# Performance work log

Hardware: AMD Instinct MI355X
Metric: run time of the kernel (lower is better)

## Reference

```python
import jax, jax.numpy as jnp
import numpy as np

NUM_BLOCKS = 16  # 4x4 grid of 2x2 blocks over the 8x8 matrix
E_BLK, H_BLK = 4, 2
E_CROSS, H_CROSS = 64, 8
VOCAB = 32000
LN_EPS = 1e-5


def _mha(x, Wqkv, bqkv, Wo, bo, nheads):
    """torch nn.MultiheadAttention (batch_first, self-attn, eval mode).
    Returns (out [B,T,E], attn weights averaged over heads [B,T,T])."""
    B, T, E = x.shape
    Dh = E // nheads
    qkv = x @ Wqkv.T + bqkv                      # [B,T,3E]
    q, k, v = jnp.split(qkv, 3, axis=-1)
    sp = lambda t: t.reshape(B, T, nheads, Dh).transpose(0, 2, 1, 3)  # [B,H,T,Dh]
    q, k, v = sp(q), sp(k), sp(v)
    scale = 1.0 / float(np.sqrt(Dh))
    scores = jnp.einsum('bhqd,bhkd->bhqk', q, k) * scale
    attn = jax.nn.softmax(scores, axis=-1)
    out = jnp.einsum('bhqk,bhkd->bhqd', attn, v).transpose(0, 2, 1, 3).reshape(B, T, E)
    return out @ Wo.T + bo, attn.mean(axis=1)


def _layernorm(x, g, b):
    mu = x.mean(-1, keepdims=True)
    var = x.var(-1, keepdims=True)
    return (x - mu) * jax.lax.rsqrt(var + LN_EPS) * g + b


def _to_blocks(M):
    # [B,T,8,8] -> [B,T,16,4]; block i = (row_blk*4+col_blk), 2x2 flattened row-major
    B, T = M.shape[:2]
    return jnp.transpose(M.reshape(B, T, 4, 2, 4, 2), (0, 1, 2, 4, 3, 5)).reshape(B, T, 16, 4)


def _from_blocks(x):
    # [B,T,16,4] -> [B,T,8,8]
    B, T = x.shape[:2]
    return jnp.transpose(x.reshape(B, T, 4, 4, 2, 2), (0, 1, 2, 4, 3, 5)).reshape(B, T, 8, 8)


def setup_inputs() -> dict:
    key = jax.random.key(0)
    ks = jax.random.split(key, 24)
    B, T = 4, 1024
    s = 0.05
    return {
        'M': jax.random.normal(ks[0], (B, T, 8, 8), jnp.float32),
        'token_ids': jax.random.randint(ks[1], (B, T), 0, VOCAB, jnp.int64),
        # 16 per-block MHA param sets (stacked)
        'Wqkv_blk': jax.random.normal(ks[2], (NUM_BLOCKS, 3 * E_BLK, E_BLK), jnp.float32) * s,
        'bqkv_blk': jnp.zeros((NUM_BLOCKS, 3 * E_BLK), jnp.float32),
        'Wo_blk': jax.random.normal(ks[3], (NUM_BLOCKS, E_BLK, E_BLK), jnp.float32) * s,
        'bo_blk': jnp.zeros((NUM_BLOCKS, E_BLK), jnp.float32),
        # cross-block MHA
        'Wqkv_c': jax.random.normal(ks[4], (3 * E_CROSS, E_CROSS), jnp.float32) * s,
        'bqkv_c': jnp.zeros((3 * E_CROSS,), jnp.float32),
        'Wo_c': jax.random.normal(ks[5], (E_CROSS, E_CROSS), jnp.float32) * s,
        'bo_c': jnp.zeros((E_CROSS,), jnp.float32),
        # FFN 64 -> 256 -> 64
        'W1': jax.random.normal(ks[6], (256, 64), jnp.float32) * s,
        'b1': jnp.zeros((256,), jnp.float32),
        'W2': jax.random.normal(ks[7], (64, 256), jnp.float32) * s,
        'b2': jnp.zeros((64,), jnp.float32),
        # LayerNorms
        'g1': jnp.ones((64,), jnp.float32), 'be1': jnp.zeros((64,), jnp.float32),
        'g2': jnp.ones((64,), jnp.float32), 'be2': jnp.zeros((64,), jnp.float32),
        # DynamicBlockSensitivity params
        'sens_emb': jax.random.normal(ks[8], (VOCAB, NUM_BLOCKS), jnp.float32) * s,
        'sens_alpha': jax.random.normal(ks[9], (NUM_BLOCKS,), jnp.float32) * s,
    }


def reference(M, token_ids, Wqkv_blk, bqkv_blk, Wo_blk, bo_blk,
              Wqkv_c, bqkv_c, Wo_c, bo_c, W1, b1, W2, b2,
              g1, be1, g2, be2, sens_emb, sens_alpha):
    B, T = M.shape[:2]
    blocks = _to_blocks(M)                                # [B,T,16,4]
    x_blk = jnp.moveaxis(blocks, 2, 0)                    # [16,B,T,4]
    blk_out, _ = jax.vmap(lambda x, W, b, Wo, bo: _mha(x, W, b, Wo, bo, H_BLK))(
        x_blk, Wqkv_blk, bqkv_blk, Wo_blk, bo_blk)        # [16,B,T,4]
    all_blocks = jnp.moveaxis(blk_out, 0, 2).reshape(B, T, 64)
    cross_out, attn_w = _mha(all_blocks, Wqkv_c, bqkv_c, Wo_c, bo_c, H_CROSS)
    all_blocks = _layernorm(all_blocks + cross_out, g1, be1)
    ffn = jax.nn.gelu(all_blocks @ W1.T + b1, approximate=False) @ W2.T + b2
    all_blocks = _layernorm(all_blocks + ffn, g2, be2)
    # Dynamic block sensitivity: token embedding + attention-received modulation
    attn_recv = attn_w.mean(axis=1)                       # [B,T] attention each token receives
    sens = jax.nn.sigmoid(sens_emb[token_ids] + attn_recv[..., None] * sens_alpha)  # [B,T,16]
    new_blocks = blocks + (all_blocks.reshape(B, T, 16, 4) - blocks) * sens[..., None]
    return _from_blocks(new_blocks)
```

## Files before the change

kernel.cpp:

```cpp
#include <hip/hip_runtime.h>
#include <hip/hip_bf16.h>
#include <math.h>

#define BB 4
#define TT 1024
#define BT 4096

#define OFF_BLOCKS 0
#define OFF_QKVB   262144
#define OFF_RECVP  262144
#define OFF_ALLB   1048576
#define OFF_QKVC   1310720
#define OFF_LC     2097152
#define OFF_ACCC   2129920
#define OFF_LN1    2396160
#define OFF_PARAMS 2658304
#define WS_FLOATS  2708624

#define P_W1T    0
#define P_W2T    16384
#define P_WQCT   32768
#define P_WOCT   45056
#define P_WOBLK  49152
#define P_BOBLK  49408
#define P_BQC    49472
#define P_BOC    49664
#define P_G1     49728
#define P_BE1    49792
#define P_B1     49856
#define P_B2     50112
#define P_G2     50176
#define P_BE2    50240
#define P_SAL    50304
#define P_TOTAL  50320

__device__ inline float rcpf(float x) { return __builtin_amdgcn_rcpf(x); }

__device__ inline float ex2(float x) {
#if __has_builtin(__builtin_amdgcn_exp2f)
  return __builtin_amdgcn_exp2f(x);
#else
  return exp2f(x);
#endif
}
__device__ inline float lg2(float x) {
#if __has_builtin(__builtin_amdgcn_logf)
  return __builtin_amdgcn_logf(x);
#else
  return __log2f(x);
#endif
}

typedef _Float16 h2 __attribute__((ext_vector_type(2)));
typedef __fp16   fh2 __attribute__((ext_vector_type(2)));
typedef _Float16 h8v __attribute__((ext_vector_type(8)));
typedef float    f4v __attribute__((ext_vector_type(4)));

__device__ inline uint pkh(float a, float b) {
#if __has_builtin(__builtin_amdgcn_cvt_pkrtz)
  fh2 r = __builtin_amdgcn_cvt_pkrtz(a, b);
  return __builtin_bit_cast(uint, r);
#else
  h2 r = { (_Float16)a, (_Float16)b };
  return __builtin_bit_cast(uint, r);
#endif
}
__device__ inline h2 toh2(uint u) { return __builtin_bit_cast(h2, u); }

__device__ inline bool detect_bf16(const void* M) {
  const unsigned short* h = (const unsigned short*)M;
  unsigned short v = h[threadIdx.x & 63];
  int e = (v >> 7) & 0xff;
  unsigned long long m = __ballot((e >= 90) && (e <= 141));
  return __popcll(m) >= 58;
}

template <bool ISBF>
__device__ inline float ldf(const void* p, int i) {
  if (ISBF) return __bfloat162float(((const __hip_bfloat16*)p)[i]);
  else      return ((const float*)p)[i];
}

template <bool ISBF>
__device__ void prep2_body(
    const void* M, const void* Wqkv_blk, const void* bqkv_blk,
    const void* W1, const void* W2, const void* Wqkv_c, const void* Wo_c,
    const void* Wo_blk, const void* bo_blk, const void* bqkv_c, const void* bo_c,
    const void* g1, const void* be1, const void* b1, const void* b2,
    const void* g2, const void* be2, const void* sens_al,
    float* blocks, float* qkv_blk, float* params) {
  if (blockIdx.x < 256) {
    int g = blockIdx.x * 256 + threadIdx.x;
    int i = g >> 12, bt = g & 4095;
    int rb = i >> 2, cb = i & 3;
    float x[4];
    #pragma unroll
    for (int r = 0; r < 2; ++r)
      #pragma unroll
      for (int c = 0; c < 2; ++c)
        x[r*2+c] = ldf<ISBF>(M, bt*64 + (rb*2+r)*8 + cb*2 + c);
    float* bo = blocks + bt*64 + i*4;
    #pragma unroll
    for (int j = 0; j < 4; ++j) bo[j] = x[j];
    float* o = qkv_blk + (i*BT + bt) * 12;
    #pragma unroll
    for (int c = 0; c < 12; ++c) {
      float a = ldf<ISBF>(bqkv_blk, i*12 + c);
      #pragma unroll
      for (int j = 0; j < 4; ++j) a += ldf<ISBF>(Wqkv_blk, i*48 + c*4 + j) * x[j];
      o[c] = a;
    }
  } else {
    for (int o = (blockIdx.x - 256)*256 + threadIdx.x; o < P_TOTAL; o += 16*256) {
      float v;
      if      (o < 16384) { int j = o >> 8, h2_ = o & 255; v = ldf<ISBF>(W1, h2_*64 + j); }
      else if (o < 32768) { int q = o - 16384; int k = q >> 6, j = q & 63; v = ldf<ISBF>(W2, j*256 + k); }
      else if (o < 45056) { int q = o - 32768; int j = q / 192, c = q % 192; v = ldf<ISBF>(Wqkv_c, c*64 + j); }
      else if (o < 49152) { int q = o - 45056; int m = q >> 6, j = q & 63; v = ldf<ISBF>(Wo_c, j*64 + m); }
      else if (o < 49408) v = ldf<ISBF>(Wo_blk, o - 49152);
      else if (o < 49472) v = ldf<ISBF>(bo_blk, o - 49408);
      else if (o < 49664) v = ldf<ISBF>(bqkv_c, o - 49472);
      else if (o < 49728) v = ldf<ISBF>(bo_c,   o - 49664);
      else if (o < 49792) v = ldf<ISBF>(g1,     o - 49728);
      else if (o < 49856) v = ldf<ISBF>(be1,    o - 49792);
      else if (o < 50112) v = ldf<ISBF>(b1,     o - 49856);
      else if (o < 50176) v = ldf<ISBF>(b2,     o - 50112);
      else if (o < 50240) v = ldf<ISBF>(g2,     o - 50176);
      else if (o < 50304) v = ldf<ISBF>(be2,    o - 50240);
      else                v = ldf<ISBF>(sens_al, o - 50304);
      params[o] = v;
    }
  }
}

__global__ void __launch_bounds__(256) k_prep3(
    const void* __restrict__ M, const void* __restrict__ Wqkv_blk,
    const void* __restrict__ bqkv_blk,
    const void* __restrict__ W1, const void* __restrict__ W2,
    const void* __restrict__ Wqkv_c, const void* __restrict__ Wo_c,
    const void* __restrict__ Wo_blk, const void* __restrict__ bo_blk,
    const void* __restrict__ bqkv_c, const void* __restrict__ bo_c,
    const void* __restrict__ g1, const void* __restrict__ be1,
    const void* __restrict__ b1, const void* __restrict__ b2,
    const void* __restrict__ g2, const void* __restrict__ be2,
    const void* __restrict__ sens_al,
    float* __restrict__ blocks, float* __restrict__ qkv_blk,
    float* __restrict__ params) {
  if (detect_bf16(M))
    prep2_body<true >(M, Wqkv_blk, bqkv_blk, W1, W2, Wqkv_c, Wo_c, Wo_blk, bo_blk,
                      bqkv_c, bo_c, g1, be1, b1, b2, g2, be2, sens_al,
                      blocks, qkv_blk, params);
  else
    prep2_body<false>(M, Wqkv_blk, bqkv_blk, W1, W2, Wqkv_c, Wo_c, Wo_blk, bo_blk,
                      bqkv_c, bo_c, g1, be1, b1, b2, g2, be2, sens_al,
                      blocks, qkv_blk, params);
}

__global__ void __launch_bounds__(1024) k_blk5(
    const float* __restrict__ qkv_blk,
    const float* __restrict__ params,
    float* __restrict__ all_blocks) {
  __shared__ __align__(16) uint lds[16916];
  uint* kvu = lds;
  uint* vt  = lds + 4096;
  ushort* vt16 = (ushort*)vt;
  int bid = blockIdx.x;
  int qg = bid & 3, b = (bid >> 2) & 3, i = bid >> 4;
  int tid = threadIdx.x;
  int wv = tid >> 6, lane = tid & 63;
  int lq = lane & 15, g = lane >> 4;
  const float* slab = qkv_blk + (size_t)(i*BT + b*TT) * 12;
  {
    int r = tid;
    const float4* rp = (const float4*)(slab + (size_t)r*12);
    float4 x1 = rp[1], x2 = rp[2];
    uint v01 = pkh(x2.x, x2.y), v23 = pkh(x2.z, x2.w);
    *(uint4*)(kvu + r*4) = make_uint4(pkh(x1.x,x1.y), pkh(x1.z,x1.w), v01, v23);
    vt16[0*1032 + r] = (ushort)(v01 & 0xffffu);
    vt16[1*1032 + r] = (ushort)(v01 >> 16);
    vt16[2*1032 + r] = (ushort)(v23 & 0xffffu);
    vt16[3*1032 + r] = (ushort)(v23 >> 16);
    vt16[4*1032 + r] = (ushort)0x3C00;
  }
  int qrow = qg*256 + wv*16 + lq;
  float4 qv = *(const float4*)(slab + (size_t)qrow*12);
  const float S2L = 0.70710678f * 1.44269504f;
  uint pq01 = pkh(qv.x*S2L, qv.y*S2L);
  uint pq23 = pkh(qv.z*S2L, qv.w*S2L);
  uint4 bq0u = make_uint4(g == 0 ? pq01 : 0u, 0u, 0u, 0u);
  uint4 bq1u = make_uint4(0u, g == 0 ? pq23 : 0u, 0u, 0u);
  h8v B0 = __builtin_bit_cast(h8v, bq0u);
  h8v B1 = __builtin_bit_cast(h8v, bq1u);
  __syncthreads();
  uint* pt0 = lds + 6676 + (size_t)(wv*2 + 0)*320;
  uint* pt1 = lds + 6676 + (size_t)(wv*2 + 1)*320;
  f4v acc0 = {0.f, 0.f, 0.f, 0.f};
  f4v acc1 = {0.f, 0.f, 0.f, 0.f};
  #pragma unroll 2
  for (int c = 0; c < 32; ++c) {
    int kb = c*32;
    #pragma unroll
    for (int t = 0; t < 2; ++t) {
      uint4 aku = *(const uint4*)(kvu + (size_t)(kb + t*16 + lq)*4);
      h8v AK = __builtin_bit_cast(h8v, aku);
      f4v z = {0.f, 0.f, 0.f, 0.f};
      f4v s0 = __builtin_amdgcn_mfma_f32_16x16x32_f16(AK, B0, z, 0, 0, 0);
      f4v s1 = __builtin_amdgcn_mfma_f32_16x16x32_f16(AK, B1, z, 0, 0, 0);
      uint a01 = pkh(ex2(s0[0]), ex2(s0[1]));
      uint a23 = pkh(ex2(s0[2]), ex2(s0[3]));
      uint c01 = pkh(ex2(s1[0]), ex2(s1[1]));
      uint c23 = pkh(ex2(s1[2]), ex2(s1[3]));
      *(uint2*)(pt0 + lq*20 + t*8 + g*2) = make_uint2(a01, a23);
      *(uint2*)(pt1 + lq*20 + t*8 + g*2) = make_uint2(c01, c23);
    }
    uint4 avu = make_uint4(0u, 0u, 0u, 0u);
    if (lq < 5) avu = *(const uint4*)(vt + (size_t)lq*516 + c*16 + g*4);
    h8v AV = __builtin_bit_cast(h8v, avu);
    h8v BP0 = __builtin_bit_cast(h8v, *(const uint4*)(pt0 + lq*20 + g*4));
    h8v BP1 = __builtin_bit_cast(h8v, *(const uint4*)(pt1 + lq*20 + g*4));
    acc0 = __builtin_amdgcn_mfma_f32_16x16x32_f16(AV, BP0, acc0, 0, 0, 0);
    acc1 = __builtin_amdgcn_mfma_f32_16x16x32_f16(AV, BP1, acc1, 0, 0, 0);
  }
  float l0 = __shfl(acc0[0], 16 + lq);
  float l1 = __shfl(acc1[0], 16 + lq);
  if (g == 0) {
    float inv0 = rcpf(l0), inv1 = rcpf(l1);
    float o[4] = { acc0[0]*inv0, acc0[1]*inv0, acc1[2]*inv1, acc1[3]*inv1 };
    const float* pWo = params + P_WOBLK + i*16;
    float4 outv;
    #pragma unroll
    for (int j = 0; j < 4; ++j) {
      float a = params[P_BOBLK + i*4 + j];
      #pragma unroll
      for (int m2 = 0; m2 < 4; ++m2) a += pWo[j*4 + m2] * o[m2];
      ((float*)&outv)[j] = a;
    }
    *(float4*)(all_blocks + (size_t)(b*TT + qrow)*64 + i*4) = outv;
  }
}

__global__ void __launch_bounds__(256) k_qkv_c3(
    const float* __restrict__ all_blocks,
    const float* __restrict__ params,
    float* __restrict__ qkv_c) {
  __shared__ __align__(16) uint wt[6912];
  int tid = threadIdx.x;
  int wv = tid >> 6, lane = tid & 63;
  int lq = lane & 15, g = lane >> 4;
  for (int o = tid; o < 6144; o += 256) {
    int c = o % 192, jp = o / 192;
    float w0 = params[P_WQCT + (2*jp    )*192 + c];
    float w1 = params[P_WQCT + (2*jp + 1)*192 + c];
    wt[c*36 + jp] = pkh(w0, w1);
  }
  int t0 = blockIdx.x * 16;
  const float* xr = all_blocks + (size_t)(t0 + lq)*64;
  uint4 a0u, a1u;
  {
    float4 x0 = *(const float4*)(xr + 8*g);
    float4 x1 = *(const float4*)(xr + 8*g + 4);
    a0u = make_uint4(pkh(x0.x,x0.y), pkh(x0.z,x0.w), pkh(x1.x,x1.y), pkh(x1.z,x1.w));
    float4 x2 = *(const float4*)(xr + 32 + 8*g);
    float4 x3 = *(const float4*)(xr + 32 + 8*g + 4);
    a1u = make_uint4(pkh(x2.x,x2.y), pkh(x2.z,x2.w), pkh(x3.x,x3.y), pkh(x3.z,x3.w));
  }
  h8v A0 = __builtin_bit_cast(h8v, a0u);
  h8v A1 = __builtin_bit_cast(h8v, a1u);
  __syncthreads();
  #pragma unroll
  for (int nt = 0; nt < 3; ++nt) {
    int ct = wv*3 + nt;
    int c = ct*16 + lq;
    h8v Bw0 = __builtin_bit_cast(h8v, *(const uint4*)(wt + c*36 + g*4));
    h8v Bw1 = __builtin_bit_cast(h8v, *(const uint4*)(wt + c*36 + 16 + g*4));
    f4v acc = {0.f, 0.f, 0.f, 0.f};
    acc = __builtin_amdgcn_mfma_f32_16x16x32_f16(A0, Bw0, acc, 0, 0, 0);
    acc = __builtin_amdgcn_mfma_f32_16x16x32_f16(A1, Bw1, acc, 0, 0, 0);
    float bias = params[P_BQC + c];
    #pragma unroll
    for (int r = 0; r < 4; ++r)
      qkv_c[(size_t)(t0 + 4*g + r)*192 + c] = acc[r] + bias;
  }
}

__global__ void __launch_bounds__(1024) k_cross12(
    const float* __restrict__ qkv_c,
    float* __restrict__ acc_c,
    float* __restrict__ recv_part) {
  __shared__ __align__(16) uint lds[24740];
  uint* Ku = lds;
  uint* Vt = lds + 4096;
  ushort* vt16 = (ushort*)Vt;
  uint* PT = lds + 8740;
  float* red = (float*)(lds + 18980);
  uint* qb_ = lds + 23716;
  float* qbf = (float*)qb_;
  int bid = blockIdx.x;
  int h = bid & 7, b = (bid >> 3) & 3, qg = bid >> 5;
  int tid = threadIdx.x;
  int wv = tid >> 6, lane = tid & 63;
  int lq = lane & 15, g = lane >> 4;
  int h8 = h*8;
  const float* base = qkv_c + (size_t)b*TT*192;
  {
    int r = tid;
    const float4* kp = (const float4*)(base + (size_t)r*192 + 64 + h8);
    const float4* vp = (const float4*)(base + (size_t)r*192 + 128 + h8);
    float4 k0 = kp[0], k1 = kp[1], v0 = vp[0], v1 = vp[1];
    *(uint4*)(Ku + r*4) = make_uint4(pkh(k0.x,k0.y), pkh(k0.z,k0.w),
                                     pkh(k1.x,k1.y), pkh(k1.z,k1.w));
    uint v01 = pkh(v0.x,v0.y), v23 = pkh(v0.z,v0.w);
    uint v45 = pkh(v1.x,v1.y), v67 = pkh(v1.z,v1.w);
    vt16[0*1032 + r] = (ushort)(v01 & 0xffffu);
    vt16[1*1032 + r] = (ushort)(v01 >> 16);
    vt16[2*1032 + r] = (ushort)(v23 & 0xffffu);
    vt16[3*1032 + r] = (ushort)(v23 >> 16);
    vt16[4*1032 + r] = (ushort)(v45 & 0xffffu);
    vt16[5*1032 + r] = (ushort)(v45 >> 16);
    vt16[6*1032 + r] = (ushort)(v67 & 0xffffu);
    vt16[7*1032 + r] = (ushort)(v67 >> 16);
    vt16[8*1032 + r] = (ushort)0x3C00;
  }
  int qpair = wv >> 2, ks = wv & 3;
  int qlA = qpair*32 + lq, qlB = qlA + 16;
  const float SCL = 0.35355339f * 1.44269504f;
  uint4 b0u = make_uint4(0u,0u,0u,0u), b1u = make_uint4(0u,0u,0u,0u);
  if (g == 0) {
    int qA = qg*128 + qlA, qB = qA + 16;
    const float4* pa = (const float4*)(base + (size_t)qA*192 + h8);
    const float4* pb = (const float4*)(base + (size_t)qB*192 + h8);
    float4 a0 = pa[0], a1 = pa[1], c0 = pb[0], c1 = pb[1];
    b0u = make_uint4(pkh(a0.x*SCL,a0.y*SCL), pkh(a0.z*SCL,a0.w*SCL),
                     pkh(a1.x*SCL,a1.y*SCL), pkh(a1.z*SCL,a1.w*SCL));
    b1u = make_uint4(pkh(c0.x*SCL,c0.y*SCL), pkh(c0.z*SCL,c0.w*SCL),
                     pkh(c1.x*SCL,c1.y*SCL), pkh(c1.z*SCL,c1.w*SCL));
    if (ks == 0) {
      *(uint4*)(qb_ + qlA*8) = b0u;
      *(uint4*)(qb_ + qlB*8) = b1u;
    }
  }
  h8v B0 = __builtin_bit_cast(h8v, b0u);
  h8v B1 = __builtin_bit_cast(h8v, b1u);
  __syncthreads();
  uint* pt0 = PT + (size_t)(wv*2)*320;
  uint* pt1 = pt0 + 320;
  f4v acc0 = {0.f,0.f,0.f,0.f};
  f4v acc1 = {0.f,0.f,0.f,0.f};
  const uint4 zu4 = make_uint4(0u,0u,0u,0u);
  for (int c = ks*8; c < ks*8 + 8; ++c) {
    #pragma unroll
    for (int t = 0; t < 2; ++t) {
      uint4 aku = (g == 0) ? *(const uint4*)(Ku + (size_t)(c*32 + t*16 + lq)*4) : zu4;
      h8v AK = __builtin_bit_cast(h8v, aku);
      f4v z = {0.f,0.f,0.f,0.f};
      f4v s0 = __builtin_amdgcn_mfma_f32_16x16x32_f16(AK, B0, z, 0, 0, 0);
      f4v s1 = __builtin_amdgcn_mfma_f32_16x16x32_f16(AK, B1, z, 0, 0, 0);
      *(uint2*)(pt0 + lq*20 + t*8 + g*2) =
          make_uint2(pkh(ex2(s0[0]), ex2(s0[1])), pkh(ex2(s0[2]), ex2(s0[3])));
      *(uint2*)(pt1 + lq*20 + t*8 + g*2) =
          make_uint2(pkh(ex2(s1[0]), ex2(s1[1])), pkh(ex2(s1[2]), ex2(s1[3])));
    }
    uint4 avu = (lq < 9) ? *(const uint4*)(Vt + (size_t)lq*516 + c*16 + g*4) : zu4;
    h8v AV = __builtin_bit_cast(h8v, avu);
    h8v BP0 = __builtin_bit_cast(h8v, *(const uint4*)(pt0 + lq*20 + g*4));
    h8v BP1 = __builtin_bit_cast(h8v, *(const uint4*)(pt1 + lq*20 + g*4));
    acc0 = __builtin_amdgcn_mfma_f32_16x16x32_f16(AV, BP0, acc0, 0, 0, 0);
    acc1 = __builtin_amdgcn_mfma_f32_16x16x32_f16(AV, BP1, acc1, 0, 0, 0);
  }
  {
    float* rA = red + (size_t)qlA*37 + ks*9;
    float* rB = red + (size_t)qlB*37 + ks*9;
    if (g == 0) {
      rA[0]=acc0[0]; rA[1]=acc0[1]; rA[2]=acc0[2]; rA[3]=acc0[3];
      rB[0]=acc1[0]; rB[1]=acc1[1]; rB[2]=acc1[2]; rB[3]=acc1[3];
    } else if (g == 1) {
      rA[4]=acc0[0]; rA[5]=acc0[1]; rA[6]=acc0[2]; rA[7]=acc0[3];
      rB[4]=acc1[0]; rB[5]=acc1[1]; rB[6]=acc1[2]; rB[7]=acc1[3];
    } else if (g == 2) {
      rA[8]=acc0[0];
      rB[8]=acc1[0];
    }
  }
  __syncthreads();
  if (tid < 128) {
    int q = tid;
    const float* rr = red + (size_t)q*37;
    float ls = rr[8] + rr[17] + rr[26] + rr[35];
    float od[8];
    #pragma unroll
    for (int d = 0; d < 8; ++d)
      od[d] = rr[d] + rr[9+d] + rr[18+d] + rr[27+d];
    float invl = rcpf(ls);
    int idx = (b*8 + h)*TT + qg*128 + q;
    float4 o0 = { od[0]*invl, od[1]*invl, od[2]*invl, od[3]*invl };
    float4 o1 = { od[4]*invl, od[5]*invl, od[6]*invl, od[7]*invl };
    float4* op = (float4*)(acc_c + (size_t)idx*8);
    op[0] = o0; op[1] = o1;
    qbf[q*8 + 4] = -lg2(ls);
  }
  __syncthreads();
  {
    int src = h*8 + qg;
    const uint4 zz = make_uint4(0u,0u,0u,0u);
    h8v  BQs[8];
    float mqs[8];
    #pragma unroll
    for (int qt = 0; qt < 8; ++qt) {
      uint4 bqu = (g == 0) ? *(const uint4*)(qb_ + (size_t)(qt*16 + lq)*8) : zz;
      BQs[qt] = __builtin_bit_cast(h8v, bqu);
      mqs[qt] = qbf[(size_t)(qt*16 + lq)*8 + 4];
    }
    #pragma unroll
    for (int it = 0; it < 4; ++it) {
      int kt = wv*4 + it;
      uint4 aku = (g == 0) ? *(const uint4*)(Ku + (size_t)(kt*16 + lq)*4) : zz;
      h8v AK = __builtin_bit_cast(h8v, aku);
      f4v racc = {0.f,0.f,0.f,0.f};
      #pragma unroll
      for (int qt = 0; qt < 8; ++qt) {
        f4v z = {0.f,0.f,0.f,0.f};
        f4v s = __builtin_amdgcn_mfma_f32_16x16x32_f16(AK, BQs[qt], z, 0, 0, 0);
        float mq = mqs[qt];
        racc[0] += ex2(s[0] + mq);
        racc[1] += ex2(s[1] + mq);
        racc[2] += ex2(s[2] + mq);
        racc[3] += ex2(s[3] + mq);
      }
      #pragma unroll
      for (int off = 1; off < 16; off <<= 1) {
        racc[0] += __shfl_xor(racc[0], off);
        racc[1] += __shfl_xor(racc[1], off);
        racc[2] += __shfl_xor(racc[2], off);
        racc[3] += __shfl_xor(racc[3], off);
      }
      if (lq == 0) {
        int k = kt*16 + g*4;
        size_t bk = ((size_t)(b*1024 + k))*64 + src;
        recv_part[bk      ] = racc[0];
        recv_part[bk +  64] = racc[1];
        recv_part[bk + 128] = racc[2];
        recv_part[bk + 192] = racc[3];
      }
    }
  }
}

template <bool ISBF>
__device__ void finffn_body(
    const float* all_blocks, const float* acc_c,
    const float* params, const float* blocks,
    const int* tok32, const float* recv_part, const void* sens_emb, void* out,
    float* w, float* ld2, float* hbuf, float* pvs) {
  int tid = threadIdx.x;
  int t0 = blockIdx.x * 8;
  int wv = tid >> 6, lane = tid & 63;
  int t = t0 + wv, b = t >> 10, tl = t & 1023;
  {
    int h = lane >> 3;
    int idx = (b*8 + h)*TT + tl;
    pvs[wv*64 + lane] = acc_c[(size_t)idx*8 + (lane & 7)];
    float a = params[P_BOC + lane];
    const float* WoT = params + P_WOCT;
    const float* p = pvs + wv*64;
    #pragma unroll 8
    for (int m = 0; m < 64; ++m) a += WoT[m*64 + lane] * p[m];
    float x = all_blocks[(size_t)t*64 + lane] + a;
    float s = x, s2 = x*x;
    #pragma unroll
    for (int off = 32; off; off >>= 1) { s += __shfl_xor(s, off); s2 += __shfl_xor(s2, off); }
    float mu  = s  * (1.f/64.f);
    float var = s2 * (1.f/64.f) - mu*mu;
    float y = (x - mu) * rsqrtf(var + 1e-5f) * params[P_G1 + lane] + params[P_BE1 + lane];
    ld2[lane*8 + wv] = y;
  }
  float recv;
  {
    int k = t & 1023;
    const float* rp = recv_part + ((size_t)(b*1024 + k))*64;
    float s = rp[lane];
    #pragma unroll
    for (int off = 32; off; off >>= 1) s += __shfl_xor(s, off);
    recv = s * (1.f/8192.f);
  }
  {
    const float4* src = (const float4*)(params + P_W1T);
    float4* dst = (float4*)w;
    #pragma unroll
    for (int i = tid; i < 4096; i += 512) dst[i] = src[i];
  }
  __syncthreads();
  {
    int g = tid >> 8, u = tid & 255;
    float a0, a1, a2, a3;
    a0 = a1 = a2 = a3 = params[P_B1 + u];
    #pragma unroll 8
    for (int j = 0; j < 64; ++j) {
      float wj = w[j*256 + u];
      float4 xj = *(const float4*)(ld2 + j*8 + g*4);
      a0 += wj*xj.x; a1 += wj*xj.y; a2 += wj*xj.z; a3 += wj*xj.w;
    }
    float av[4] = {a0, a1, a2, a3};
    float4 hv;
    #pragma unroll
    for (int t2 = 0; t2 < 4; ++t2) {
      float v = av[t2];
      float u2 = 1.5957691f*v + 0.07135481f*v*v*v;
      ((float*)&hv)[t2] = v * rcpf(1.f + __expf(-u2));
    }
    *(float4*)(hbuf + u*8 + g*4) = hv;
  }
  __syncthreads();
  {
    const float4* src = (const float4*)(params + P_W2T);
    float4* dst = (float4*)w;
    #pragma unroll
    for (int i = tid; i < 4096; i += 512) dst[i] = src[i];
  }
  __syncthreads();
  float yp[8] = {0.f,0.f,0.f,0.f,0.f,0.f,0.f,0.f};
  {
    int j = lane, k0 = wv*32;
    #pragma unroll 8
    for (int k = k0; k < k0 + 32; ++k) {
      float wkj = w[k*64 + j];
      float4 h03 = *(const float4*)(hbuf + k*8);
      float4 h47 = *(const float4*)(hbuf + k*8 + 4);
      yp[0] += wkj*h03.x; yp[1] += wkj*h03.y; yp[2] += wkj*h03.z; yp[3] += wkj*h03.w;
      yp[4] += wkj*h47.x; yp[5] += wkj*h47.y; yp[6] += wkj*h47.z; yp[7] += wkj*h47.w;
    }
  }
  __syncthreads();
  float* red2 = w;
  {
    #pragma unroll
    for (int t2 = 0; t2 < 8; ++t2) red2[wv*520 + t2*64 + lane] = yp[t2];
  }
  __syncthreads();
  int j = lane;
  int tok = wv;
  float y = params[P_B2 + j];
  #pragma unroll
  for (int wq = 0; wq < 8; ++wq) y += red2[wq*520 + tok*64 + j];
  float z = ld2[j*8 + tok] + y;
  float s = z, s2 = z*z;
  #pragma unroll
  for (int off = 32; off; off >>= 1) { s += __shfl_xor(s, off); s2 += __shfl_xor(s2, off); }
  float mu  = s  * (1.f/64.f);
  float var = s2 * (1.f/64.f) - mu*mu;
  float y2 = (z - mu) * rsqrtf(var + 1e-5f) * params[P_G2 + j] + params[P_BE2 + j];
  bool is64 = ((tok32[1] | tok32[3] | tok32[5] | tok32[7]) == 0);
  int tk = is64 ? tok32[t*2] : tok32[t];
  int i = j >> 2, e = j & 3;
  float sv = ldf<ISBF>(sens_emb, tk*16 + i) + recv * params[P_SAL + i];
  float sg = rcpf(1.f + __expf(-sv));
  float blk = blocks[t*64 + j];
  float nb = blk + (y2 - blk) * sg;
  int rb = i >> 2, cb = i & 3, r = e >> 1, c = e & 1;
  int oidx = t*64 + (rb*2 + r)*8 + cb*2 + c;
  if (ISBF) ((__hip_bfloat16*)out)[oidx] = __float2bfloat16(nb);
  else      ((float*)out)[oidx] = nb;
}

__global__ void __launch_bounds__(512) k_finffn(
    const void* __restrict__ M,
    const float* __restrict__ all_blocks,
    const float* __restrict__ acc_c,
    const float* __restrict__ params,
    const float* __restrict__ blocks,
    const int* __restrict__ tok32,
    const float* __restrict__ recv_part,
    const void* __restrict__ sens_emb,
    void* __restrict__ out) {
  __shared__ float w[16384];
  __shared__ float ld2[512];
  __shared__ float hbuf[2048];
  __shared__ float pvs[512];
  if (detect_bf16(M))
    finffn_body<true >(all_blocks, acc_c, params, blocks, tok32, recv_part,
                       sens_emb, out, w, ld2, hbuf, pvs);
  else
    finffn_body<false>(all_blocks, acc_c, params, blocks, tok32, recv_part,
                       sens_emb, out, w, ld2, hbuf, pvs);
}

extern "C" void kernel_launch(void* const* d_in, const int* in_sizes, int n_in,
                              void* d_out, int out_size, void* d_ws, size_t ws_size,
                              hipStream_t stream) {
  const void* M        = d_in[0];
  const int*  tok      = (const int*)d_in[1];
  const void* Wqkv_blk = d_in[2];
  const void* bqkv_blk = d_in[3];
  const void* Wo_blk   = d_in[4];
  const void* bo_blk   = d_in[5];
  const void* Wqkv_c   = d_in[6];
  const void* bqkv_c   = d_in[7];
  const void* Wo_c     = d_in[8];
  const void* bo_c     = d_in[9];
  const void* W1       = d_in[10];
  const void* b1       = d_in[11];
  const void* W2       = d_in[12];
  const void* b2       = d_in[13];
  const void* g1       = d_in[14];
  const void* be1      = d_in[15];
  const void* g2i      = d_in[16];
  const void* be2      = d_in[17];
  const void* sens_emb = d_in[18];
  const void* sens_al  = d_in[19];

  float* ws = (float*)d_ws;
  float* blocks    = ws + OFF_BLOCKS;
  float* qkv_blk   = ws + OFF_QKVB;
  float* recv_part = ws + OFF_RECVP;
  float* all_blk   = ws + OFF_ALLB;
  float* qkv_c     = ws + OFF_QKVC;
  float* acc_c     = ws + OFF_ACCC;
  float* params    = ws + OFF_PARAMS;

  k_prep3<<<272, 256, 0, stream>>>(M, Wqkv_blk, bqkv_blk, W1, W2, Wqkv_c, Wo_c,
                                   Wo_blk, bo_blk, bqkv_c, bo_c, g1, be1, b1, b2,
                                   g2i, be2, sens_al, blocks, qkv_blk, params);
  k_blk5<<<256, 1024, 0, stream>>>(qkv_blk, params, all_blk);
  k_qkv_c3<<<256, 256, 0, stream>>>(all_blk, params, qkv_c);
  k_cross12<<<256, 1024, 0, stream>>>(qkv_c, acc_c, recv_part);
  k_finffn<<<512, 512, 0, stream>>>(M, all_blk, acc_c, params, blocks, tok,
                                    recv_part, sens_emb, (void*)d_out);
}
```

Baseline: 166.5 us.

## Fuse per-block QKV projection into block attention kernel, drop qkv_blk buffer

The per-block QKV projection and block gather move out of the prep kernel and into the block attention kernel. Each workgroup now reads M directly and computes K/V for its 1024 rows and Q for its own rows. This removes the write and reread of the 12-float qkv_blk intermediate and shrinks the prep kernel to 16 workgroups of parameter transposition. In exchange, each of the four query-group workgroups recomputes K/V for the same rows, and M is read redundantly with strided 2x2 access.

```diff
diff --git a/kernel.cpp b/kernel.cpp
--- a/kernel.cpp
+++ b/kernel.cpp
@@ -82,60 +82,35 @@
 }
 
 template <bool ISBF>
-__device__ void prep2_body(
-    const void* M, const void* Wqkv_blk, const void* bqkv_blk,
+__device__ void prep4_body(
     const void* W1, const void* W2, const void* Wqkv_c, const void* Wo_c,
     const void* Wo_blk, const void* bo_blk, const void* bqkv_c, const void* bo_c,
     const void* g1, const void* be1, const void* b1, const void* b2,
     const void* g2, const void* be2, const void* sens_al,
-    float* blocks, float* qkv_blk, float* params) {
-  if (blockIdx.x < 256) {
-    int g = blockIdx.x * 256 + threadIdx.x;
-    int i = g >> 12, bt = g & 4095;
-    int rb = i >> 2, cb = i & 3;
-    float x[4];
-    #pragma unroll
-    for (int r = 0; r < 2; ++r)
-      #pragma unroll
-      for (int c = 0; c < 2; ++c)
-        x[r*2+c] = ldf<ISBF>(M, bt*64 + (rb*2+r)*8 + cb*2 + c);
-    float* bo = blocks + bt*64 + i*4;
-    #pragma unroll
-    for (int j = 0; j < 4; ++j) bo[j] = x[j];
-    float* o = qkv_blk + (i*BT + bt) * 12;
-    #pragma unroll
-    for (int c = 0; c < 12; ++c) {
-      float a = ldf<ISBF>(bqkv_blk, i*12 + c);
-      #pragma unroll
-      for (int j = 0; j < 4; ++j) a += ldf<ISBF>(Wqkv_blk, i*48 + c*4 + j) * x[j];
-      o[c] = a;
-    }
-  } else {
-    for (int o = (blockIdx.x - 256)*256 + threadIdx.x; o < P_TOTAL; o += 16*256) {
-      float v;
-      if      (o < 16384) { int j = o >> 8, h2_ = o & 255; v = ldf<ISBF>(W1, h2_*64 + j); }
-      else if (o < 32768) { int q = o - 16384; int k = q >> 6, j = q & 63; v = ldf<ISBF>(W2, j*256 + k); }
-      else if (o < 45056) { int q = o - 32768; int j = q / 192, c = q % 192; v = ldf<ISBF>(Wqkv_c, c*64 + j); }
-      else if (o < 49152) { int q = o - 45056; int m = q >> 6, j = q & 63; v = ldf<ISBF>(Wo_c, j*64 + m); }
-      else if (o < 49408) v = ldf<ISBF>(Wo_blk, o - 49152);
-      else if (o < 49472) v = ldf<ISBF>(bo_blk, o - 49408);
-      else if (o < 49664) v = ldf<ISBF>(bqkv_c, o - 49472);
-      else if (o < 49728) v = ldf<ISBF>(bo_c,   o - 49664);
-      else if (o < 49792) v = ldf<ISBF>(g1,     o - 49728);
-      else if (o < 49856) v = ldf<ISBF>(be1,    o - 49792);
-      else if (o < 50112) v = ldf<ISBF>(b1,     o - 49856);
-      else if (o < 50176) v = ldf<ISBF>(b2,     o - 50112);
-      else if (o < 50240) v = ldf<ISBF>(g2,     o - 50176);
-      else if (o < 50304) v = ldf<ISBF>(be2,    o - 50240);
-      else                v = ldf<ISBF>(sens_al, o - 50304);
-      params[o] = v;
-    }
-  }
-}
-
-__global__ void __launch_bounds__(256) k_prep3(
-    const void* __restrict__ M, const void* __restrict__ Wqkv_blk,
-    const void* __restrict__ bqkv_blk,
+    float* params) {
+  for (int o = blockIdx.x*256 + threadIdx.x; o < P_TOTAL; o += 16*256) {
+    float v;
+    if      (o < 16384) { int j = o >> 8, h2_ = o & 255; v = ldf<ISBF>(W1, h2_*64 + j); }
+    else if (o < 32768) { int q = o - 16384; int k = q >> 6, j = q & 63; v = ldf<ISBF>(W2, j*256 + k); }
+    else if (o < 45056) { int q = o - 32768; int j = q / 192, c = q % 192; v = ldf<ISBF>(Wqkv_c, c*64 + j); }
+    else if (o < 49152) { int q = o - 45056; int m = q >> 6, j = q & 63; v = ldf<ISBF>(Wo_c, j*64 + m); }
+    else if (o < 49408) v = ldf<ISBF>(Wo_blk, o - 49152);
+    else if (o < 49472) v = ldf<ISBF>(bo_blk, o - 49408);
+    else if (o < 49664) v = ldf<ISBF>(bqkv_c, o - 49472);
+    else if (o < 49728) v = ldf<ISBF>(bo_c,   o - 49664);
+    else if (o < 49792) v = ldf<ISBF>(g1,     o - 49728);
+    else if (o < 49856) v = ldf<ISBF>(be1,    o - 49792);
+    else if (o < 50112) v = ldf<ISBF>(b1,     o - 49856);
+    else if (o < 50176) v = ldf<ISBF>(b2,     o - 50112);
+    else if (o < 50240) v = ldf<ISBF>(g2,     o - 50176);
+    else if (o < 50304) v = ldf<ISBF>(be2,    o - 50240);
+    else                v = ldf<ISBF>(sens_al, o - 50304);
+    params[o] = v;
+  }
+}
+
+__global__ void __launch_bounds__(256) k_prep4(
+    const void* __restrict__ M,
     const void* __restrict__ W1, const void* __restrict__ W2,
     const void* __restrict__ Wqkv_c, const void* __restrict__ Wo_c,
     const void* __restrict__ Wo_blk, const void* __restrict__ bo_blk,
@@ -144,23 +119,19 @@
     const void* __restrict__ b1, const void* __restrict__ b2,
     const void* __restrict__ g2, const void* __restrict__ be2,
     const void* __restrict__ sens_al,
-    float* __restrict__ blocks, float* __restrict__ qkv_blk,
     float* __restrict__ params) {
   if (detect_bf16(M))
-    prep2_body<true >(M, Wqkv_blk, bqkv_blk, W1, W2, Wqkv_c, Wo_c, Wo_blk, bo_blk,
-                      bqkv_c, bo_c, g1, be1, b1, b2, g2, be2, sens_al,
-                      blocks, qkv_blk, params);
+    prep4_body<true >(W1, W2, Wqkv_c, Wo_c, Wo_blk, bo_blk, bqkv_c, bo_c,
+                      g1, be1, b1, b2, g2, be2, sens_al, params);
   else
-    prep2_body<false>(M, Wqkv_blk, bqkv_blk, W1, W2, Wqkv_c, Wo_c, Wo_blk, bo_blk,
-                      bqkv_c, bo_c, g1, be1, b1, b2, g2, be2, sens_al,
-                      blocks, qkv_blk, params);
-}
-
-__global__ void __launch_bounds__(1024) k_blk5(
-    const float* __restrict__ qkv_blk,
-    const float* __restrict__ params,
-    float* __restrict__ all_blocks) {
-  __shared__ __align__(16) uint lds[16916];
+    prep4_body<false>(W1, W2, Wqkv_c, Wo_c, Wo_blk, bo_blk, bqkv_c, bo_c,
+                      g1, be1, b1, b2, g2, be2, sens_al, params);
+}
+
+template <bool ISBF>
+__device__ void blk6_body(
+    const void* M, const void* Wqkv_blk, const void* bqkv_blk,
+    const float* params, float* blocks, float* all_blocks, uint* lds) {
   uint* kvu = lds;
   uint* vt  = lds + 4096;
   ushort* vt16 = (ushort*)vt;
@@ -169,13 +140,41 @@
   int tid = threadIdx.x;
   int wv = tid >> 6, lane = tid & 63;
   int lq = lane & 15, g = lane >> 4;
-  const float* slab = qkv_blk + (size_t)(i*BT + b*TT) * 12;
+  int rb = i >> 2, cb = i & 3;
+  float Wk[4][4], Wv[4][4], bk[4], bv[4];
+  #pragma unroll
+  for (int c = 0; c < 4; ++c) {
+    bk[c] = ldf<ISBF>(bqkv_blk, i*12 + 4 + c);
+    bv[c] = ldf<ISBF>(bqkv_blk, i*12 + 8 + c);
+    #pragma unroll
+    for (int j = 0; j < 4; ++j) {
+      Wk[c][j] = ldf<ISBF>(Wqkv_blk, i*48 + (4+c)*4 + j);
+      Wv[c][j] = ldf<ISBF>(Wqkv_blk, i*48 + (8+c)*4 + j);
+    }
+  }
   {
     int r = tid;
-    const float4* rp = (const float4*)(slab + (size_t)r*12);
-    float4 x1 = rp[1], x2 = rp[2];
-    uint v01 = pkh(x2.x, x2.y), v23 = pkh(x2.z, x2.w);
-    *(uint4*)(kvu + r*4) = make_uint4(pkh(x1.x,x1.y), pkh(x1.z,x1.w), v01, v23);
+    size_t mb = (size_t)(b*TT + r)*64;
+    float x[4];
+    #pragma unroll
+    for (int rr = 0; rr < 2; ++rr)
+      #pragma unroll
+      for (int cc = 0; cc < 2; ++cc)
+        x[rr*2+cc] = ldf<ISBF>(M, mb + (rb*2+rr)*8 + cb*2 + cc);
+    if (qg == 0) {
+      float4 bx = { x[0], x[1], x[2], x[3] };
+      *(float4*)(blocks + mb + i*4) = bx;
+    }
+    float kk[4], vv[4];
+    #pragma unroll
+    for (int c = 0; c < 4; ++c) {
+      float ak = bk[c], av = bv[c];
+      #pragma unroll
+      for (int j = 0; j < 4; ++j) { ak += Wk[c][j]*x[j]; av += Wv[c][j]*x[j]; }
+      kk[c] = ak; vv[c] = av;
+    }
+    uint v01 = pkh(vv[0], vv[1]), v23 = pkh(vv[2], vv[3]);
+    *(uint4*)(kvu + r*4) = make_uint4(pkh(kk[0],kk[1]), pkh(kk[2],kk[3]), v01, v23);
     vt16[0*1032 + r] = (ushort)(v01 & 0xffffu);
     vt16[1*1032 + r] = (ushort)(v01 >> 16);
     vt16[2*1032 + r] = (ushort)(v23 & 0xffffu);
@@ -183,10 +182,26 @@
     vt16[4*1032 + r] = (ushort)0x3C00;
   }
   int qrow = qg*256 + wv*16 + lq;
-  float4 qv = *(const float4*)(slab + (size_t)qrow*12);
+  float q[4];
+  {
+    size_t mb = (size_t)(b*TT + qrow)*64;
+    float x[4];
+    #pragma unroll
+    for (int rr = 0; rr < 2; ++rr)
+      #pragma unroll
+      for (int cc = 0; cc < 2; ++cc)
+        x[rr*2+cc] = ldf<ISBF>(M, mb + (rb*2+rr)*8 + cb*2 + cc);
+    #pragma unroll
+    for (int c = 0; c < 4; ++c) {
+      float a = ldf<ISBF>(bqkv_blk, i*12 + c);
+      #pragma unroll
+      for (int j = 0; j < 4; ++j) a += ldf<ISBF>(Wqkv_blk, i*48 + c*4 + j) * x[j];
+      q[c] = a;
+    }
+  }
   const float S2L = 0.70710678f * 1.44269504f;
-  uint pq01 = pkh(qv.x*S2L, qv.y*S2L);
-  uint pq23 = pkh(qv.z*S2L, qv.w*S2L);
+  uint pq01 = pkh(q[0]*S2L, q[1]*S2L);
+  uint pq23 = pkh(q[2]*S2L, q[3]*S2L);
   uint4 bq0u = make_uint4(g == 0 ? pq01 : 0u, 0u, 0u, 0u);
   uint4 bq1u = make_uint4(0u, g == 0 ? pq23 : 0u, 0u, 0u);
   h8v B0 = __builtin_bit_cast(h8v, bq0u);
@@ -237,6 +252,20 @@
     }
     *(float4*)(all_blocks + (size_t)(b*TT + qrow)*64 + i*4) = outv;
   }
+}
+
+__global__ void __launch_bounds__(1024) k_blk6(
+    const void* __restrict__ M,
+    const void* __restrict__ Wqkv_blk,
+    const void* __restrict__ bqkv_blk,
+    const float* __restrict__ params,
+    float* __restrict__ blocks,
+    float* __restrict__ all_blocks) {
+  __shared__ __align__(16) uint lds[16916];
+  if (detect_bf16(M))
+    blk6_body<true >(M, Wqkv_blk, bqkv_blk, params, blocks, all_blocks, lds);
+  else
+    blk6_body<false>(M, Wqkv_blk, bqkv_blk, params, blocks, all_blocks, lds);
 }
 
 __global__ void __launch_bounds__(256) k_qkv_c3(
@@ -609,17 +638,16 @@
 
   float* ws = (float*)d_ws;
   float* blocks    = ws + OFF_BLOCKS;
-  float* qkv_blk   = ws + OFF_QKVB;
   float* recv_part = ws + OFF_RECVP;
   float* all_blk   = ws + OFF_ALLB;
   float* qkv_c     = ws + OFF_QKVC;
   float* acc_c     = ws + OFF_ACCC;
   float* params    = ws + OFF_PARAMS;
 
-  k_prep3<<<272, 256, 0, stream>>>(M, Wqkv_blk, bqkv_blk, W1, W2, Wqkv_c, Wo_c,
-                                   Wo_blk, bo_blk, bqkv_c, bo_c, g1, be1, b1, b2,
-                                   g2i, be2, sens_al, blocks, qkv_blk, params);
-  k_blk5<<<256, 1024, 0, stream>>>(qkv_blk, params, all_blk);
+  k_prep4<<<16, 256, 0, stream>>>(M, W1, W2, Wqkv_c, Wo_c, Wo_blk, bo_blk,
+                                  bqkv_c, bo_c, g1, be1, b1, b2, g2i, be2,
+                                  sens_al, params);
+  k_blk6<<<256, 1024, 0, stream>>>(M, Wqkv_blk, bqkv_blk, params, blocks, all_blk);
   k_qkv_c3<<<256, 256, 0, stream>>>(all_blk, params, qkv_c);
   k_cross12<<<256, 1024, 0, stream>>>(qkv_c, acc_c, recv_part);
   k_finffn<<<512, 512, 0, stream>>>(M, all_blk, acc_c, params, blocks, tok,
```

Result: slower. 171.9 us (+3.2%).
